# Kernel tuning notes

Hardware: AMD Instinct MI355X
Metric: run time of the kernel (lower is better)

Reference implementation:

```python
import jax, jax.numpy as jnp
import numpy as np


def setup_inputs() -> dict:
    key = jax.random.key(0)
    ks = jax.random.split(key, 7)
    B, S, V_, E, H, C = 64, 2048, 50257, 128, 256, 2
    x = jax.random.randint(ks[0], (B, S), 0, V_, dtype=jnp.int64)
    emb = jax.random.normal(ks[1], (V_, E), dtype=jnp.float32) * 0.02
    W = jax.random.normal(ks[2], (E, H), dtype=jnp.float32) * (1.0 / np.sqrt(E))
    U = jax.random.normal(ks[3], (H, H), dtype=jnp.float32) * (1.0 / np.sqrt(H))
    bU = jax.random.normal(ks[4], (H,), dtype=jnp.float32) * 0.02
    V = jax.random.normal(ks[5], (H, C), dtype=jnp.float32) * (1.0 / np.sqrt(H))
    bV = jax.random.normal(ks[6], (C,), dtype=jnp.float32) * 0.02
    return {"x": x, "emb": emb, "W": W, "U": U, "bU": bU, "V": V, "bV": bV}


def reference(x, emb, W, U, bU, V, bV):
    # padding_idx=0: row 0 of the embedding table is zeros
    emb_eff = emb.at[0].set(0.0)
    embedded = emb_eff[x]                      # [B, S, E]
    B = x.shape[0]
    H = U.shape[0]
    h0 = jnp.zeros((B, H), dtype=embedded.dtype)
    # precompute input projections for all steps in one GEMM: [B,S,H] -> scan over S
    xw = jnp.einsum('bse,eh->sbh', embedded, W)  # [S, B, H]

    def step(h, xw_t):
        h = jnp.tanh(xw_t + h @ U + bU)
        return h, None

    h, _ = jax.lax.scan(step, h0, xw)
    output = h @ V + bV                        # [B, num_classes]
    return (output, h)
```

## Files before the change

### kernel.cpp

```cpp
#include <hip/hip_runtime.h>
#include <hip/hip_bf16.h>


#define HB 256
#define EB 128
#define SB 2048
#define BB 64
#define TPB 32
#define ROWS 4
#define PITCH 272

typedef unsigned short u16;
typedef __attribute__((ext_vector_type(4))) float f32x4;
typedef __attribute__((ext_vector_type(8))) _Float16 f16x8;
typedef __attribute__((ext_vector_type(2))) __fp16 fp16x2_t;

__device__ __forceinline__ u16 f2h_bits(float f) {
    union { _Float16 h; u16 b; } x; x.h = (_Float16)f; return x.b;
}
__device__ __forceinline__ float h2f_bits(u16 b) {
    union { u16 b; _Float16 h; } x; x.b = b; return (float)x.h;
}
__device__ __forceinline__ float tanh_fast(float z) {
    float E = exp2f(z * 2.885390082f);
    return fmaf(-2.f, __builtin_amdgcn_rcpf(E + 1.f), 1.f);
}
__device__ __forceinline__ unsigned pkrtz(float a, float b) {
    fp16x2_t p = __builtin_amdgcn_cvt_pkrtz(a, b);
    return __builtin_bit_cast(unsigned, p);
}
__device__ __forceinline__ float sel4(f32x4 v, int kg) {
    float r = v[0];
    r = (kg == 1) ? v[1] : r;
    r = (kg == 2) ? v[2] : r;
    r = (kg == 3) ? v[3] : r;
    return r;
}

__device__ __forceinline__ int sig(int j)    { return (j & 0xE0) | ((j & 15) << 1) | ((j >> 4) & 1); }
__device__ __forceinline__ int invsig(int p) { return (p & 0xE0) | ((p & 1) << 4) | ((p >> 1) & 15); }

__global__ __launch_bounds__(256) void embed_proj(
    const int* __restrict__ x, const float* __restrict__ emb,
    const float* __restrict__ W, const float* __restrict__ bU,
    u16* __restrict__ xw)
{
    __shared__ __align__(16) float el[TPB][EB];
    __shared__ int toks[TPB];

    const int tid = threadIdx.x;
    const long base = (long)blockIdx.x * TPB;

    if (tid < TPB) toks[tid] = x[base + tid];
    __syncthreads();

    for (int r = 0; r < TPB * EB / 256; ++r) {
        int i = tid + r * 256;
        int row = i >> 7, e = i & (EB - 1);
        int u = toks[row];
        el[row][e] = (u == 0) ? 0.f : emb[(size_t)u * EB + e];
    }
    __syncthreads();

    const int j = tid;
    const int sj = sig(j);
    const float bu = bU[j];
    float acc[TPB];
    #pragma unroll
    for (int t = 0; t < TPB; ++t) acc[t] = bu;

    for (int e0 = 0; e0 < EB; e0 += 4) {
        float w0 = W[(e0 + 0) * HB + j];
        float w1 = W[(e0 + 1) * HB + j];
        float w2 = W[(e0 + 2) * HB + j];
        float w3 = W[(e0 + 3) * HB + j];
        #pragma unroll
        for (int t = 0; t < TPB; ++t) {
            float4 ev = *(const float4*)&el[t][e0];
            acc[t] = fmaf(ev.x, w0, acc[t]);
            acc[t] = fmaf(ev.y, w1, acc[t]);
            acc[t] = fmaf(ev.z, w2, acc[t]);
            acc[t] = fmaf(ev.w, w3, acc[t]);
        }
    }
    #pragma unroll
    for (int t = 0; t < TPB; ++t)
        xw[(base + t) * HB + sj] = f2h_bits(acc[t]);
}

#define STEP(T, X)                                                                 \
  {                                                                                \
    const int cb = (T) & 1, nb = cb ^ 1;                                           \
    float xv0 = h2f_bits((u16)(X & 0xffffu));                                      \
    float xv1 = h2f_bits((u16)(X >> 16));                                          \
    f32x4 acc0 = {xv0, xv0, xv0, xv0};                                             \
    f32x4 acc1 = {xv1, xv1, xv1, xv1};                                             \
    {                                                                              \
        const unsigned toff = (unsigned)(((T) + 2 < SB) ? (T) + 2 : SB - 1) * HB;  \
        X = *(const unsigned*)&xw[gb + toff];                                      \
    }                                                                              \
    f16x8 Af[8];                                                                   \
    _Pragma("unroll")                                                              \
    for (int ks = 0; ks < 8; ++ks) {                                               \
        uint4 av = *(const uint4*)&H[cb][n & 3][ks * 32 + kg * 8];                 \
        Af[ks] = __builtin_bit_cast(f16x8, av);                                    \
    }                                                                              \
    _Pragma("unroll")                                                              \
    for (int ks = 0; ks < 8; ++ks) {                                               \
        acc0 = __builtin_amdgcn_mfma_f32_16x16x32_f16(Af[ks], Bf[0][ks], acc0, 0, 0, 0); \
        acc1 = __builtin_amdgcn_mfma_f32_16x16x32_f16(Af[ks], Bf[1][ks], acc1, 0, 0, 0); \
    }                                                                              \
    {                                                                              \
        float t0 = tanh_fast(sel4(acc0, kg));                                      \
        float t1 = tanh_fast(sel4(acc1, kg));                                      \
        *(unsigned*)&H[nb][kg][pbase] = pkrtz(t0, t1);                             \
    }                                                                              \
    __syncthreads();                                                               \
  }

__global__ __launch_bounds__(512, 2) void rnn_scan_mfma(
    const u16* __restrict__ xw, const float* __restrict__ U,
    const float* __restrict__ V, const float* __restrict__ bV,
    float* __restrict__ out)
{
    __shared__ __align__(16) u16 H[2][ROWS][PITCH];

    const int tid  = threadIdx.x;
    const int lane = tid & 63;
    const int w    = tid >> 6;
    const int b0   = blockIdx.x * ROWS;

    {
        unsigned* hz = (unsigned*)H;
        for (int i = tid; i < 2 * ROWS * PITCH / 2; i += 512) hz[i] = 0u;
    }

    const int n  = lane & 15;
    const int kg = lane >> 4;

    f16x8 Bf[2][8];
    #pragma unroll
    for (int s = 0; s < 2; ++s) {
        const int col = (2 * w + s) * 16 + n;
        #pragma unroll
        for (int ks = 0; ks < 8; ++ks) {
            union { f16x8 v; u16 h[8]; } tmp;
            #pragma unroll
            for (int e = 0; e < 8; ++e) {
                const int p = ks * 32 + kg * 8 + e;
                const int jin = invsig(p);
                tmp.h[e] = f2h_bits(U[(size_t)jin * HB + col]);
            }
            Bf[s][ks] = tmp.v;
        }
    }

    const int pbase = 32 * w + 2 * n;
    const unsigned gb = ((unsigned)(b0 + kg) * SB) * HB + pbase;
    unsigned XA = *(const unsigned*)&xw[gb];
    unsigned XB = *(const unsigned*)&xw[gb + HB];
    __syncthreads();

    for (int t = 0; t < SB; t += 2) {
        STEP(t,     XA);
        STEP(t + 1, XB);
    }

    for (int i = tid; i < ROWS * HB; i += 512) {
        const int r = i >> 8, p = i & 255;
        out[BB * 2 + (size_t)(b0 + r) * HB + invsig(p)] = h2f_bits(H[0][r][p]);
    }

    if (tid < ROWS * 16) {
        const int r = tid >> 4, part = tid & 15;
        float s0 = 0.f, s1 = 0.f;
        #pragma unroll
        for (int i = 0; i < 16; ++i) {
            const int p = part * 16 + i;
            const int j = invsig(p);
            float hh = h2f_bits(H[0][r][p]);
            s0 = fmaf(hh, V[j * 2 + 0], s0);
            s1 = fmaf(hh, V[j * 2 + 1], s1);
        }
        #pragma unroll
        for (int o = 8; o > 0; o >>= 1) {
            s0 += __shfl_down(s0, o, 16);
            s1 += __shfl_down(s1, o, 16);
        }
        if (part == 0) {
            out[(size_t)(b0 + r) * 2 + 0] = s0 + bV[0];
            out[(size_t)(b0 + r) * 2 + 1] = s1 + bV[1];
        }
    }
}

extern "C" void kernel_launch(void* const* d_in, const int* in_sizes, int n_in,
                              void* d_out, int out_size, void* d_ws, size_t ws_size,
                              hipStream_t stream) {
    const int*   x   = (const int*)d_in[0];
    const float* emb = (const float*)d_in[1];
    const float* W   = (const float*)d_in[2];
    const float* U   = (const float*)d_in[3];
    const float* bU  = (const float*)d_in[4];
    const float* V   = (const float*)d_in[5];
    const float* bV  = (const float*)d_in[6];
    float* out = (float*)d_out;
    u16*   xw  = (u16*)d_ws;

    embed_proj<<<BB * SB / TPB, 256, 0, stream>>>(x, emb, W, bU, xw);
    rnn_scan_mfma<<<BB / ROWS, 512, 0, stream>>>(xw, U, V, bV, out);
}
```

Measured before the change: 1.065 ms.

## Rewrite embedding projection with fp16 MFMA on 64-token tiles

The embedding-gather plus projection kernel now packs gathered embedding rows to fp16 in LDS and runs the x·W projection with 16x16x32 fp16 MFMA instructions, replacing the scalar FMA loop. Each block now covers 64 tokens, and W fragments are loaded into registers once per block. Outputs are written as packed fp16 pairs in the permuted column order the scan kernel expects. This cuts ALU time in the projection stage, but the embedding inputs are now rounded to fp16, and the sequential scan kernel probably still dominates total time.

```diff
diff --git a/kernel.cpp b/kernel.cpp
--- a/kernel.cpp
+++ b/kernel.cpp
@@ -6,7 +6,8 @@
 #define EB 128
 #define SB 2048
 #define BB 64
-#define TPB 32
+#define ETPB 64
+#define APITCH 68
 #define ROWS 4
 #define PITCH 272
 
@@ -28,6 +29,9 @@
 __device__ __forceinline__ unsigned pkrtz(float a, float b) {
     fp16x2_t p = __builtin_amdgcn_cvt_pkrtz(a, b);
     return __builtin_bit_cast(unsigned, p);
+}
+__device__ __forceinline__ unsigned pkrne(float a, float b) {
+    return (unsigned)f2h_bits(a) | ((unsigned)f2h_bits(b) << 16);
 }
 __device__ __forceinline__ float sel4(f32x4 v, int kg) {
     float r = v[0];
@@ -40,52 +44,80 @@
 __device__ __forceinline__ int sig(int j)    { return (j & 0xE0) | ((j & 15) << 1) | ((j >> 4) & 1); }
 __device__ __forceinline__ int invsig(int p) { return (p & 0xE0) | ((p & 1) << 4) | ((p >> 1) & 15); }
 
-__global__ __launch_bounds__(256) void embed_proj(
+__global__ __launch_bounds__(256) void embed_proj_mfma(
     const int* __restrict__ x, const float* __restrict__ emb,
     const float* __restrict__ W, const float* __restrict__ bU,
     u16* __restrict__ xw)
 {
-    __shared__ __align__(16) float el[TPB][EB];
-    __shared__ int toks[TPB];
+    __shared__ int toks[ETPB];
+    __shared__ __align__(16) unsigned el[ETPB * APITCH];
 
     const int tid = threadIdx.x;
-    const long base = (long)blockIdx.x * TPB;
-
-    if (tid < TPB) toks[tid] = x[base + tid];
+    const long base = (long)blockIdx.x * ETPB;
+    if (tid < ETPB) toks[tid] = x[base + tid];
     __syncthreads();
 
-    for (int r = 0; r < TPB * EB / 256; ++r) {
-        int i = tid + r * 256;
-        int row = i >> 7, e = i & (EB - 1);
+    #pragma unroll
+    for (int r = 0; r < ETPB * 64 / 256; ++r) {
+        int idx = tid + r * 256;
+        int row = idx >> 6, ep = idx & 63;
         int u = toks[row];
-        el[row][e] = (u == 0) ? 0.f : emb[(size_t)u * EB + e];
+        unsigned pk = 0u;
+        if (u != 0) {
+            float2 v = *(const float2*)&emb[(size_t)u * EB + 2 * ep];
+            pk = pkrne(v.x, v.y);
+        }
+        el[row * APITCH + ep] = pk;
+    }
+
+    const int lane = tid & 63;
+    const int w    = tid >> 6;
+    const int n    = lane & 15;
+    const int kg   = lane >> 4;
+
+    f16x8 Bf[4][4];
+    float bu[4];
+    #pragma unroll
+    for (int s = 0; s < 4; ++s) {
+        const int col = (4 * w + s) * 16 + n;
+        bu[s] = bU[col];
+        #pragma unroll
+        for (int ks = 0; ks < 4; ++ks) {
+            union { f16x8 v; u16 h[8]; } tmp;
+            #pragma unroll
+            for (int e = 0; e < 8; ++e)
+                tmp.h[e] = f2h_bits(W[(size_t)(ks * 32 + kg * 8 + e) * HB + col]);
+            Bf[s][ks] = tmp.v;
+        }
     }
     __syncthreads();
 
-    const int j = tid;
-    const int sj = sig(j);
-    const float bu = bU[j];
-    float acc[TPB];
-    #pragma unroll
-    for (int t = 0; t < TPB; ++t) acc[t] = bu;
-
-    for (int e0 = 0; e0 < EB; e0 += 4) {
-        float w0 = W[(e0 + 0) * HB + j];
-        float w1 = W[(e0 + 1) * HB + j];
-        float w2 = W[(e0 + 2) * HB + j];
-        float w3 = W[(e0 + 3) * HB + j];
-        #pragma unroll
-        for (int t = 0; t < TPB; ++t) {
-            float4 ev = *(const float4*)&el[t][e0];
-            acc[t] = fmaf(ev.x, w0, acc[t]);
-            acc[t] = fmaf(ev.y, w1, acc[t]);
-            acc[t] = fmaf(ev.z, w2, acc[t]);
-            acc[t] = fmaf(ev.w, w3, acc[t]);
-        }
-    }
-    #pragma unroll
-    for (int t = 0; t < TPB; ++t)
-        xw[(base + t) * HB + sj] = f2h_bits(acc[t]);
+    #pragma unroll
+    for (int mt = 0; mt < 4; ++mt) {
+        f16x8 Af[4];
+        #pragma unroll
+        for (int ks = 0; ks < 4; ++ks) {
+            uint4 av = *(const uint4*)&el[(mt * 16 + n) * APITCH + ks * 16 + kg * 4];
+            Af[ks] = __builtin_bit_cast(f16x8, av);
+        }
+        f32x4 acc0 = {bu[0], bu[0], bu[0], bu[0]};
+        f32x4 acc1 = {bu[1], bu[1], bu[1], bu[1]};
+        f32x4 acc2 = {bu[2], bu[2], bu[2], bu[2]};
+        f32x4 acc3 = {bu[3], bu[3], bu[3], bu[3]};
+        #pragma unroll
+        for (int ks = 0; ks < 4; ++ks) {
+            acc0 = __builtin_amdgcn_mfma_f32_16x16x32_f16(Af[ks], Bf[0][ks], acc0, 0, 0, 0);
+            acc1 = __builtin_amdgcn_mfma_f32_16x16x32_f16(Af[ks], Bf[1][ks], acc1, 0, 0, 0);
+            acc2 = __builtin_amdgcn_mfma_f32_16x16x32_f16(Af[ks], Bf[2][ks], acc2, 0, 0, 0);
+            acc3 = __builtin_amdgcn_mfma_f32_16x16x32_f16(Af[ks], Bf[3][ks], acc3, 0, 0, 0);
+        }
+        #pragma unroll
+        for (int q = 0; q < 4; ++q) {
+            const long tok = base + mt * 16 + kg * 4 + q;
+            *(unsigned*)&xw[tok * HB + 64 * w + 2 * n]      = pkrne(acc0[q], acc1[q]);
+            *(unsigned*)&xw[tok * HB + 64 * w + 32 + 2 * n] = pkrne(acc2[q], acc3[q]);
+        }
+    }
 }
 
 #define STEP(T, X)                                                                 \
@@ -207,6 +239,6 @@
     float* out = (float*)d_out;
     u16*   xw  = (u16*)d_ws;
 
-    embed_proj<<<BB * SB / TPB, 256, 0, stream>>>(x, emb, W, bU, xw);
+    embed_proj_mfma<<<BB * SB / ETPB, 256, 0, stream>>>(x, emb, W, bU, xw);
     rnn_scan_mfma<<<BB / ROWS, 512, 0, stream>>>(xw, U, V, bV, out);
 }
```

New measurement: 943.0 us. -11.4%, faster.
